# Kernel optimization log

Measured on AMD Instinct MI355X. Metric: run time of the kernel, lower is better.

The kernel has to match this reference:

```python
import jax, jax.numpy as jnp
import numpy as np

BS, N, XC, K, YS = 64, 1024, 1024, 256, 768

def setup_inputs() -> dict:
    key = jax.random.key(0)
    ks = jax.random.split(key, 5)
    return {
        "x": jax.random.normal(ks[0], (BS, N, XC), dtype=jnp.float32),
        "y": jax.random.normal(ks[1], (BS, YS), dtype=jnp.float32),
        "W_ch": jax.random.normal(ks[2], (K, XC), dtype=jnp.float32) * 0.02,
        "b_ch": jax.random.normal(ks[3], (K,), dtype=jnp.float32) * 0.02,
        "W_y": jax.random.normal(ks[4], (K, YS), dtype=jnp.float32) * 0.02,
    }

def reference(x, y, W_ch, b_ch, W_y):
    # y_k: [bs, k] (no bias)
    y_k = jnp.einsum('bs,ks->bk', y, W_y)
    # channel affine on every spatial position, batched: [bs, n, k]
    x_k = jnp.einsum('bnc,kc->bnk', x, W_ch) + b_ch
    # add per-sample y_k (broadcast over spatial dim), tanh, softmax over k
    z = jnp.tanh(x_k + y_k[:, None, :])
    attn = jax.nn.softmax(z, axis=-1)
    # torch.cat over dim=0 of per-sample [n, k] blocks -> [bs*n, k]
    return attn.reshape(-1, attn.shape[-1])
```

## Files before the change

kernel.cpp:

```cpp
#include <hip/hip_runtime.h>


#define XC    1024
#define KOUT  256
#define NT    16
#define LDSZ  65536

typedef float        f32x4_t  __attribute__((ext_vector_type(4)));
typedef unsigned int u32x4_t  __attribute__((ext_vector_type(4)));
typedef unsigned int u32x2_t  __attribute__((ext_vector_type(2)));
typedef __bf16       bf16x8_t __attribute__((ext_vector_type(8)));

__device__ __forceinline__ unsigned short f2bf(float f) {
  unsigned int u = __float_as_uint(f);
  u += 0x7fffu + ((u >> 16) & 1u);
  return (unsigned short)(u >> 16);
}

__device__ __forceinline__ float fast_tanh(float v) {
  float e = __expf(2.0f * v);
  return 1.0f - 2.0f / (e + 1.0f);
}

#define LGKM_BARRIER() do {                                  \
    asm volatile("s_waitcnt lgkmcnt(0)" ::: "memory");       \
    __builtin_amdgcn_s_barrier();                            \
    __builtin_amdgcn_sched_barrier(0);                       \
  } while (0)

__global__ void prep_kernel(const float* __restrict__ Wch,
                            const float* __restrict__ y,
                            const float* __restrict__ Wy,
                            const float* __restrict__ bch,
                            unsigned short* __restrict__ wbf,
                            float* __restrict__ biasws) {
  if (blockIdx.x < 256) {
    const int k = blockIdx.x;
    const int u = threadIdx.x;
    f32x4_t v = ((const f32x4_t*)(Wch + k * XC))[u];
    const int c0   = u << 2;
    const int t    = c0 >> 6;
    const int ch   = (c0 & 63) >> 3;
    const int kk   = ch >> 2;
    const int lg   = ch & 3;
    const int half = (c0 >> 2) & 1;
    const int wv   = k >> 6;
    const int ni   = (k >> 4) & 3;
    const int lr   = k & 15;
    const int lane = (lg << 4) | lr;
    unsigned int lo = (unsigned int)f2bf(v.x) | ((unsigned int)f2bf(v.y) << 16);
    unsigned int hi = (unsigned int)f2bf(v.z) | ((unsigned int)f2bf(v.w) << 16);
    char* p = (char*)wbf +
              ((size_t)((((t << 2) + wv) * 2 + kk) * 4 + ni) << 10) +
              (lane << 4) + (half << 3);
    *(u32x2_t*)p = (u32x2_t){lo, hi};
  } else {
    __shared__ __align__(16) float ys[768];
    const int b = blockIdx.x - 256;
    const int k = threadIdx.x;
    for (int i = k; i < 768; i += 256) ys[i] = y[b * 768 + i];
    __syncthreads();
    const f32x4_t* w4 = (const f32x4_t*)(Wy + k * 768);
    const f32x4_t* y4 = (const f32x4_t*)ys;
    float s = 0.f;
#pragma unroll 8
    for (int i = 0; i < 192; ++i) {
      f32x4_t w = w4[i], a = y4[i];
      s = fmaf(w.x, a.x, s); s = fmaf(w.y, a.y, s);
      s = fmaf(w.z, a.z, s); s = fmaf(w.w, a.w, s);
    }
    biasws[b * 256 + k] = s + bch[k];
  }
}

__global__ __launch_bounds__(256, 2) void fused_kernel(
    const float* __restrict__ x, const unsigned short* __restrict__ wbf,
    const float* __restrict__ bias, float* __restrict__ out) {
  __shared__ __align__(16) unsigned char smem[LDSZ];
  const int tid = threadIdx.x;
  const int l   = tid & 63;
  const int w   = tid >> 6;
  const int lr  = l & 15;
  const int lg  = l >> 4;
  const int m0  = blockIdx.x << 5;
  const int bidx = m0 >> 10;
  const int t0  = blockIdx.x & 15;

  f32x4_t acc[2][4];
#pragma unroll
  for (int i = 0; i < 2; ++i)
#pragma unroll
    for (int j = 0; j < 4; ++j) acc[i][j] = (f32x4_t){0.f, 0.f, 0.f, 0.f};

  const f32x4_t* xbase = (const f32x4_t*)(x + (size_t)m0 * XC);
  const char* wsrc = (const char*)wbf + (w << 13) + (l << 4);
  f32x4_t G0[8], G1[8];
  bf16x8_t bfrA[8], bfrB[8];

#define LOADG(dst, i0) do {                                                  \
    _Pragma("unroll")                                                        \
    for (int j = 0; j < 8; ++j)                                              \
      dst[j] = xbase[(size_t)((i0) + j) * 256 + tid];                        \
  } while (0)

#define WRITEG(src, i0) do {                                                 \
    _Pragma("unroll")                                                        \
    for (int j = 0; j < 8; ++j) {                                            \
      const int row = (i0) + j;                                              \
      unsigned int lo = (unsigned int)f2bf(src[j].x) |                       \
                        ((unsigned int)f2bf(src[j].y) << 16);                \
      unsigned int hi = (unsigned int)f2bf(src[j].z) |                       \
                        ((unsigned int)f2bf(src[j].w) << 16);                \
      char* p = (char*)smem + ((tid >> 4) << 12) + row * 128 +               \
                ((((tid & 15) >> 1) ^ (row & 7)) << 4) + ((tid & 1) << 3);   \
      *(u32x2_t*)p = (u32x2_t){lo, hi};                                      \
    }                                                                        \
  } while (0)

#define LOADB(dst, tt) do {                                                  \
    const char* g = wsrc + (size_t)(tt) * 32768;                             \
    _Pragma("unroll")                                                        \
    for (int f = 0; f < 8; ++f)                                              \
      dst[f] = __builtin_bit_cast(bf16x8_t, *(const u32x4_t*)(g + (f << 10)));\
  } while (0)

#define COMPUTE_T(tt, bsrc) do {                                             \
    const u32x4_t* aB = (const u32x4_t*)(smem + ((tt) << 12));               \
    _Pragma("unroll")                                                        \
    for (int kk = 0; kk < 2; ++kk) {                                         \
      const int cs = ((kk << 2) | lg) ^ (lr & 7);                            \
      bf16x8_t afr[2];                                                       \
      _Pragma("unroll")                                                      \
      for (int mi = 0; mi < 2; ++mi)                                         \
        afr[mi] = __builtin_bit_cast(bf16x8_t, aB[(((mi << 4) + lr) << 3) + cs]);\
      _Pragma("unroll")                                                      \
      for (int mi = 0; mi < 2; ++mi)                                         \
        _Pragma("unroll")                                                    \
        for (int nj = 0; nj < 4; ++nj)                                       \
          acc[mi][nj] = __builtin_amdgcn_mfma_f32_16x16x32_bf16(             \
              afr[mi], bsrc[(kk << 2) | nj], acc[mi][nj], 0, 0, 0);          \
    }                                                                        \
  } while (0)

  LOADG(G0, 0);
  LOADG(G1, 8);
  WRITEG(G0, 0);
  LOADG(G0, 16);
  WRITEG(G1, 8);
  LOADG(G1, 24);
  WRITEG(G0, 16);
  WRITEG(G1, 24);
  LOADB(bfrA, t0);
  LGKM_BARRIER();

#pragma unroll
  for (int s = 0; s < NT; s += 2) {
    LOADB(bfrB, ((s + 1 + t0) & 15));
    COMPUTE_T(((s + t0) & 15), bfrA);
    if (s + 2 < NT) LOADB(bfrA, ((s + 2 + t0) & 15));
    COMPUTE_T(((s + 1 + t0) & 15), bfrB);
  }
  __syncthreads();

#undef LOADG
#undef WRITEG
#undef LOADB
#undef COMPUTE_T

  float* wred    = (float*)smem;
  float* rowstat = (float*)(smem + 512);

  float brow[4];
#pragma unroll
  for (int ni = 0; ni < 4; ++ni)
    brow[ni] = bias[(bidx << 8) + (w << 6) + (ni << 4) + lr];

#pragma unroll
  for (int mi = 0; mi < 2; ++mi)
#pragma unroll
    for (int ni = 0; ni < 4; ++ni)
#pragma unroll
      for (int r = 0; r < 4; ++r)
        acc[mi][ni][r] = fast_tanh(acc[mi][ni][r] + brow[ni]);

#pragma unroll
  for (int mi = 0; mi < 2; ++mi)
#pragma unroll
    for (int r = 0; r < 4; ++r) {
      float m = fmaxf(fmaxf(acc[mi][0][r], acc[mi][1][r]),
                      fmaxf(acc[mi][2][r], acc[mi][3][r]));
      m = fmaxf(m, __shfl_xor(m, 1));
      m = fmaxf(m, __shfl_xor(m, 2));
      m = fmaxf(m, __shfl_xor(m, 4));
      m = fmaxf(m, __shfl_xor(m, 8));
      if (lr == 0) wred[(w << 5) + (mi << 4) + (lg << 2) + r] = m;
    }
  __syncthreads();
  if (tid < 32)
    rowstat[tid] = fmaxf(fmaxf(wred[tid], wred[32 + tid]),
                         fmaxf(wred[64 + tid], wred[96 + tid]));
  __syncthreads();

#pragma unroll
  for (int mi = 0; mi < 2; ++mi)
#pragma unroll
    for (int r = 0; r < 4; ++r) {
      const int row = (mi << 4) + (lg << 2) + r;
      const float m = rowstat[row];
      float s = 0.f;
#pragma unroll
      for (int ni = 0; ni < 4; ++ni) {
        float e = __expf(acc[mi][ni][r] - m);
        acc[mi][ni][r] = e;
        s += e;
      }
      s += __shfl_xor(s, 1);
      s += __shfl_xor(s, 2);
      s += __shfl_xor(s, 4);
      s += __shfl_xor(s, 8);
      if (lr == 0) wred[(w << 5) + row] = s;
    }
  __syncthreads();
  if (tid < 32)
    rowstat[tid] = 1.0f / (wred[tid] + wred[32 + tid] +
                           wred[64 + tid] + wred[96 + tid]);
  __syncthreads();

#pragma unroll
  for (int mi = 0; mi < 2; ++mi)
#pragma unroll
    for (int r = 0; r < 4; ++r) {
      const int row = (mi << 4) + (lg << 2) + r;
      const float rinv = rowstat[row];
      float* orow = out + (size_t)(m0 + row) * KOUT + (w << 6) + lr;
#pragma unroll
      for (int ni = 0; ni < 4; ++ni)
        orow[ni << 4] = acc[mi][ni][r] * rinv;
    }
}

extern "C" void kernel_launch(void* const* d_in, const int* in_sizes, int n_in,
                              void* d_out, int out_size, void* d_ws, size_t ws_size,
                              hipStream_t stream) {
  (void)in_sizes; (void)n_in; (void)out_size; (void)ws_size;
  const float* x   = (const float*)d_in[0];
  const float* y   = (const float*)d_in[1];
  const float* Wch = (const float*)d_in[2];
  const float* bch = (const float*)d_in[3];
  const float* Wy  = (const float*)d_in[4];
  float* out = (float*)d_out;
  unsigned short* wbf = (unsigned short*)d_ws;
  float* biasws = (float*)((char*)d_ws + 512 * 1024);

  hipLaunchKernelGGL(prep_kernel, dim3(320), dim3(256), 0, stream,
                     Wch, y, Wy, bch, wbf, biasws);
  hipLaunchKernelGGL(fused_kernel, dim3(2048), dim3(256), 0, stream,
                     x, wbf, biasws, out);
}
```

Before: 138.4 us.

## Stream x panel in quarters with double-buffered LDS to raise occupancy

The kernel no longer stages the whole 32x1024 bf16 A panel in 64KB of LDS up front. It now loads the panel in four K-quarters into two 16KB ping-pong buffers, overlapping global loads and bf16 conversion of the next quarter with MFMA on the current one. Halving LDS lets launch bounds ask for 3 blocks per CU, which hides memory latency better. The cost is extra barriers per quarter and more register pressure under the tighter launch bound, which could cause spills.

```diff
diff --git a/kernel.cpp b/kernel.cpp
--- a/kernel.cpp
+++ b/kernel.cpp
@@ -3,8 +3,7 @@
 
 #define XC    1024
 #define KOUT  256
-#define NT    16
-#define LDSZ  65536
+#define LDSZ  32768
 
 typedef float        f32x4_t  __attribute__((ext_vector_type(4)));
 typedef unsigned int u32x4_t  __attribute__((ext_vector_type(4)));
@@ -73,7 +72,7 @@
   }
 }
 
-__global__ __launch_bounds__(256, 2) void fused_kernel(
+__global__ __launch_bounds__(256, 3) void fused_kernel(
     const float* __restrict__ x, const unsigned short* __restrict__ wbf,
     const float* __restrict__ bias, float* __restrict__ out) {
   __shared__ __align__(16) unsigned char smem[LDSZ];
@@ -84,7 +83,7 @@
   const int lg  = l >> 4;
   const int m0  = blockIdx.x << 5;
   const int bidx = m0 >> 10;
-  const int t0  = blockIdx.x & 15;
+  const int r0  = blockIdx.x & 3;
 
   f32x4_t acc[2][4];
 #pragma unroll
@@ -92,40 +91,41 @@
 #pragma unroll
     for (int j = 0; j < 4; ++j) acc[i][j] = (f32x4_t){0.f, 0.f, 0.f, 0.f};
 
-  const f32x4_t* xbase = (const f32x4_t*)(x + (size_t)m0 * XC);
-  const char* wsrc = (const char*)wbf + (w << 13) + (l << 4);
-  f32x4_t G0[8], G1[8];
+  const char* xpanel = (const char*)x + ((size_t)m0 << 12);
+  const char* wsrc   = (const char*)wbf + (w << 13) + (l << 4);
+  f32x4_t G[8];
   bf16x8_t bfrA[8], bfrB[8];
 
-#define LOADG(dst, i0) do {                                                  \
+#define LOADG(qp) do {                                                       \
     _Pragma("unroll")                                                        \
     for (int j = 0; j < 8; ++j)                                              \
-      dst[j] = xbase[(size_t)((i0) + j) * 256 + tid];                        \
-  } while (0)
-
-#define WRITEG(src, i0) do {                                                 \
+      G[j] = *(const f32x4_t*)(xpanel + (size_t)((j << 2) + w) * 4096 +      \
+                               ((qp) << 10) + (l << 4));                     \
+  } while (0)
+
+#define WRITEG(buf) do {                                                     \
     _Pragma("unroll")                                                        \
     for (int j = 0; j < 8; ++j) {                                            \
-      const int row = (i0) + j;                                              \
-      unsigned int lo = (unsigned int)f2bf(src[j].x) |                       \
-                        ((unsigned int)f2bf(src[j].y) << 16);                \
-      unsigned int hi = (unsigned int)f2bf(src[j].z) |                       \
-                        ((unsigned int)f2bf(src[j].w) << 16);                \
-      char* p = (char*)smem + ((tid >> 4) << 12) + row * 128 +               \
-                ((((tid & 15) >> 1) ^ (row & 7)) << 4) + ((tid & 1) << 3);   \
+      const int row = (j << 2) + w;                                          \
+      unsigned int lo = (unsigned int)f2bf(G[j].x) |                         \
+                        ((unsigned int)f2bf(G[j].y) << 16);                  \
+      unsigned int hi = (unsigned int)f2bf(G[j].z) |                         \
+                        ((unsigned int)f2bf(G[j].w) << 16);                  \
+      char* p = (char*)smem + ((buf) << 14) + ((l >> 4) << 12) + row * 128 + \
+                ((((l & 15) >> 1) ^ (row & 7)) << 4) + ((l & 1) << 3);       \
       *(u32x2_t*)p = (u32x2_t){lo, hi};                                      \
     }                                                                        \
   } while (0)
 
-#define LOADB(dst, tt) do {                                                  \
-    const char* g = wsrc + (size_t)(tt) * 32768;                             \
+#define LOADB(dst, tg) do {                                                  \
+    const char* g = wsrc + (size_t)(tg) * 32768;                             \
     _Pragma("unroll")                                                        \
     for (int f = 0; f < 8; ++f)                                              \
       dst[f] = __builtin_bit_cast(bf16x8_t, *(const u32x4_t*)(g + (f << 10)));\
   } while (0)
 
-#define COMPUTE_T(tt, bsrc) do {                                             \
-    const u32x4_t* aB = (const u32x4_t*)(smem + ((tt) << 12));               \
+#define COMPUTE(buf, tl, bsrc) do {                                          \
+    const u32x4_t* aB = (const u32x4_t*)(smem + ((buf) << 14) + ((tl) << 12));\
     _Pragma("unroll")                                                        \
     for (int kk = 0; kk < 2; ++kk) {                                         \
       const int cs = ((kk << 2) | lg) ^ (lr & 7);                            \
@@ -142,30 +142,41 @@
     }                                                                        \
   } while (0)
 
-  LOADG(G0, 0);
-  LOADG(G1, 8);
-  WRITEG(G0, 0);
-  LOADG(G0, 16);
-  WRITEG(G1, 8);
-  LOADG(G1, 24);
-  WRITEG(G0, 16);
-  WRITEG(G1, 24);
-  LOADB(bfrA, t0);
+#define QP(q)   (((q) + r0) & 3)
+#define TG(q,s) ((QP(q) << 2) | (s))
+
+#define QUARTER(q) do {                                                      \
+    if ((q) > 0) { WRITEG((q) & 1); LGKM_BARRIER(); }                        \
+    LOADB(bfrB, TG(q, 1));                                                   \
+    if ((q) < 3) LOADG(QP((q) + 1));                                         \
+    COMPUTE((q) & 1, 0, bfrA);                                               \
+    LOADB(bfrA, TG(q, 2));                                                   \
+    COMPUTE((q) & 1, 1, bfrB);                                               \
+    LOADB(bfrB, TG(q, 3));                                                   \
+    COMPUTE((q) & 1, 2, bfrA);                                               \
+    if ((q) < 3) LOADB(bfrA, TG((q) + 1, 0));                                \
+    COMPUTE((q) & 1, 3, bfrB);                                               \
+  } while (0)
+
+  LOADG(QP(0));
+  LOADB(bfrA, TG(0, 0));
+  WRITEG(0);
   LGKM_BARRIER();
 
-#pragma unroll
-  for (int s = 0; s < NT; s += 2) {
-    LOADB(bfrB, ((s + 1 + t0) & 15));
-    COMPUTE_T(((s + t0) & 15), bfrA);
-    if (s + 2 < NT) LOADB(bfrA, ((s + 2 + t0) & 15));
-    COMPUTE_T(((s + 1 + t0) & 15), bfrB);
-  }
+  QUARTER(0);
+  QUARTER(1);
+  QUARTER(2);
+  QUARTER(3);
+
   __syncthreads();
 
 #undef LOADG
 #undef WRITEG
 #undef LOADB
-#undef COMPUTE_T
+#undef COMPUTE
+#undef QP
+#undef TG
+#undef QUARTER
 
   float* wred    = (float*)smem;
   float* rowstat = (float*)(smem + 512);
```

Measured after the change: 130.4 us. 5.8% less time.
